# Performance work log

Measured on AMD Instinct MI355X. Metric: run time of the kernel, lower is better.

Reference implementation:

```python
import jax, jax.numpy as jnp
import numpy as np

N = 100000      # nodes
E = 3200000     # edges (before self-loops)
F_IN = 512      # input feature dim
HEADS = 8
DIM = 8         # per-head dim for hidden layers
HID = HEADS * DIM  # 64
CLS = 40        # num_classes
NEG_SLOPE = 0.2 # PyG GATConv default leaky relu slope


def setup_inputs() -> dict:
    key = jax.random.key(0)
    ks = jax.random.split(key, 14)
    def glorot(k, shape, fan_in):
        return jax.random.normal(k, shape, jnp.float32) * (1.0 / np.sqrt(fan_in))
    return {
        "x": jax.random.normal(ks[0], (N, F_IN), jnp.float32),
        "edge_index": jax.random.randint(ks[1], (2, E), 0, N, dtype=jnp.int32),
        # layer 1: in=F_IN, heads=8, dim=8, concat
        "W1": glorot(ks[2], (F_IN, HEADS * DIM), F_IN),
        "a_src1": glorot(ks[3], (HEADS, DIM), DIM),
        "a_dst1": glorot(ks[4], (HEADS, DIM), DIM),
        "b1": jnp.zeros((HEADS * DIM,), jnp.float32),
        # layer 2: in=64, heads=8, dim=8, concat
        "W2": glorot(ks[5], (HID, HEADS * DIM), HID),
        "a_src2": glorot(ks[6], (HEADS, DIM), DIM),
        "a_dst2": glorot(ks[7], (HEADS, DIM), DIM),
        "b2": jnp.zeros((HEADS * DIM,), jnp.float32),
        # layer 3: in=64, heads=1, dim=CLS, no concat (mean over heads == identity)
        "W3": glorot(ks[8], (HID, CLS), HID),
        "a_src3": glorot(ks[9], (1, CLS), CLS),
        "a_dst3": glorot(ks[10], (1, CLS), CLS),
        "b3": jnp.zeros((CLS,), jnp.float32),
    }


def gat_layer(h_in, W, att_src, att_dst, bias, src, dst, heads, dim, concat):
    # h_in: [N, F], W: [F, heads*dim], att_*: [heads, dim]
    n = h_in.shape[0]
    h = (h_in @ W).reshape(n, heads, dim)                    # [N, H, D]
    a_s = jnp.sum(h * att_src, axis=-1)                      # [N, H]
    a_d = jnp.sum(h * att_dst, axis=-1)                      # [N, H]
    e = jax.nn.leaky_relu(a_s[src] + a_d[dst], NEG_SLOPE)    # [E', H] edge logits
    # segment-softmax over incoming edges of each dst node (self-loops guarantee non-empty)
    m = jax.ops.segment_max(e, dst, num_segments=n)          # [N, H]
    p = jnp.exp(e - m[dst])
    s = jax.ops.segment_sum(p, dst, num_segments=n)          # [N, H]
    alpha = p / s[dst]                                       # [E', H]
    out = jax.ops.segment_sum(alpha[:, :, None] * h[src], dst, num_segments=n)  # [N, H, D]
    out = out.reshape(n, heads * dim) if concat else out.mean(axis=1)
    return out + bias


def reference(x, edge_index, W1, a_src1, a_dst1, b1, W2, a_src2, a_dst2, b2, W3, a_src3, a_dst3, b3):
    # PyG GATConv default add_self_loops=True
    loops = jnp.arange(N, dtype=edge_index.dtype)
    src = jnp.concatenate([edge_index[0], loops])
    dst = jnp.concatenate([edge_index[1], loops])
    h = gat_layer(x, W1, a_src1, a_dst1, b1, src, dst, HEADS, DIM, True)
    h = jax.nn.elu(h)  # dropout inactive in eval mode
    h = gat_layer(h, W2, a_src2, a_dst2, b2, src, dst, HEADS, DIM, True)
    h = jax.nn.elu(h)
    h = gat_layer(h, W3, a_src3, a_dst3, b3, src, dst, 1, CLS, False)
    return jax.nn.log_softmax(h, axis=1)
```

## Files before the change

kernel.cpp:

```cpp
#include <hip/hip_runtime.h>
#include <math.h>

#define NN 100000
#define EE 3200000
#define ET 3300000
#define FIN 512
#define HDIM 64
#define NCLS 40

#define NBUK 512
#define NPB 196
#define NBUK_USED 511
#define EPB 4096
#define EPT 16
#define CAP 8192

typedef __attribute__((ext_vector_type(8))) short frag_ab;
typedef __attribute__((ext_vector_type(4))) float frag_cd;

__device__ inline unsigned short f2bf(float f){
  union { float f; unsigned int u; } x; x.f = f;
  unsigned int u = x.u;
  unsigned int r = u + 0x7FFF + ((u >> 16) & 1);
  return (unsigned short)(r >> 16);
}
__device__ inline float bflo(unsigned u){
  union { unsigned u; float f; } x; x.u = u << 16; return x.f;
}
__device__ inline float bfhi(unsigned u){
  union { unsigned u; float f; } x; x.u = u & 0xFFFF0000u; return x.f;
}
__device__ inline float bf2f(unsigned short u){
  union { unsigned int u; float f; } x; x.u = ((unsigned int)u) << 16;
  return x.f;
}

__global__ void k_zeroB(int* bcur){
  int t = blockIdx.x*256 + threadIdx.x;
  if(t < NBUK) bcur[t] = 0;
}

__global__ __launch_bounds__(256) void k_bucket(const int* __restrict__ src, const int* __restrict__ dst,
                                                int* __restrict__ bcur, int* __restrict__ pbuf){
  __shared__ int lcnt[NBUK];
  __shared__ int lbase[NBUK];
  int t = threadIdx.x;
  for(int i=t;i<NBUK;i+=256) lcnt[i]=0;
  __syncthreads();
  int base = blockIdx.x*EPB + t;
  int bk[EPT], rk[EPT], pk[EPT];
  #pragma unroll
  for(int j=0;j<EPT;j++){
    int e = base + j*256;
    bk[j] = -1;
    if(e < ET){
      int s, d;
      if(e < EE){ s = src[e]; d = dst[e]; } else { s = e - EE; d = s; }
      int b = d / NPB;
      bk[j] = b;
      pk[j] = s | ((d - b*NPB) << 17);
      rk[j] = atomicAdd(&lcnt[b], 1);
    }
  }
  __syncthreads();
  for(int i=t;i<NBUK;i+=256){
    int v = lcnt[i];
    lbase[i] = v ? atomicAdd(&bcur[i], v) : 0;
  }
  __syncthreads();
  #pragma unroll
  for(int j=0;j<EPT;j++){
    if(bk[j] >= 0){
      int pos = lbase[bk[j]] + rk[j];
      if(pos < CAP) pbuf[(size_t)bk[j]*CAP + pos] = pk[j];
    }
  }
}

__global__ void k_bscan(const int* __restrict__ bcur, int* __restrict__ bbase){
  __shared__ int lds[NBUK];
  int t = threadIdx.x;
  int v = (t < NBUK_USED) ? bcur[t] : 0;
  lds[t] = v;
  __syncthreads();
  for(int off=1; off<NBUK; off<<=1){
    int x = 0;
    if(t >= off) x = lds[t-off];
    __syncthreads();
    if(t >= off) lds[t] += x;
    __syncthreads();
  }
  bbase[t] = lds[t] - v;
}

__global__ __launch_bounds__(256) void k_bfinal(const int* __restrict__ bbase, const int* __restrict__ pbuf,
                                                int* __restrict__ rp, int* __restrict__ col){
  __shared__ int cnt[NPB];
  int b = blockIdx.x, t = threadIdx.x;
  int beg = bbase[b];
  int cntb = bbase[b+1] - beg;
  const int* pb = pbuf + (size_t)b*CAP;
  for(int i=t;i<NPB;i+=256) cnt[i]=0;
  __syncthreads();
  for(int i=t; i<cntb; i+=256){
    int dloc = pb[i] >> 17;
    atomicAdd(&cnt[dloc], 1);
  }
  __syncthreads();
  if(t < 64){
    int vals[4]; int sum = 0;
    #pragma unroll
    for(int j=0;j<4;j++){ int idx = t*4+j; int v = (idx<NPB)?cnt[idx]:0; vals[j]=v; sum+=v; }
    int incl = sum;
    #pragma unroll
    for(int off=1; off<64; off<<=1){
      int x = __shfl_up(incl, off);
      if(t >= off) incl += x;
    }
    int run = incl - sum;
    #pragma unroll
    for(int j=0;j<4;j++){
      int idx = t*4+j;
      if(idx < NPB){ int v = vals[j]; cnt[idx] = run; run += v; }
    }
  }
  __syncthreads();
  int node0 = b*NPB;
  int nloc = NN - node0; if(nloc > NPB) nloc = NPB;
  for(int i=t;i<nloc;i+=256){
    int g = beg + cnt[i];
    rp[node0 + i] = g;
    cnt[i] = g;
  }
  if(b == 0 && t == 0) rp[NN] = ET;
  __syncthreads();
  for(int i=t; i<cntb; i+=256){
    int v = pb[i];
    int s = v & 0x1FFFF;
    int dloc = v >> 17;
    int pos = atomicAdd(&cnt[dloc], 1);
    col[pos] = s;
  }
}

__global__ void k_cvtW(const float* __restrict__ W, unsigned short* __restrict__ Wt, int K, int C){
  int i = blockIdx.x*256 + threadIdx.x;
  if(i >= 64*K) return;
  int n = i / K, k = i - n*K;
  Wt[i] = (n < C) ? f2bf(W[k*C + n]) : (unsigned short)0;
}

#define BM 128
#define BK 32
#define LSTR 40
__global__ __launch_bounds__(256) void k_gemm1(const float* __restrict__ A, const unsigned short* __restrict__ Wt,
                                               unsigned short* __restrict__ Out, int M){
  __shared__ __attribute__((aligned(16))) unsigned short Al[2][BM*LSTR];
  __shared__ __attribute__((aligned(16))) unsigned short Bl[2][64*LSTR];
  int t = threadIdx.x;
  int w = t >> 6, l = t & 63;
  int row0 = blockIdx.x * BM;

  int srow = t >> 1;
  int shalf = t & 1;
  int bn = t >> 2;
  int bseg = t & 3;

  int fr = l & 15, kg = l >> 4;

  frag_cd acc[2][4];
  #pragma unroll
  for(int i=0;i<2;i++)
    #pragma unroll
    for(int j=0;j<4;j++) acc[i][j] = (frag_cd){0.f,0.f,0.f,0.f};

  int rg = row0 + srow; if(rg >= M) rg = M-1;
  const float* aprow = &A[(size_t)rg*FIN + shalf*16];

  #define STAGE(buf, kc) do { \
    const float* ap = aprow + (kc); \
    float4 v0 = *(const float4*)(ap); \
    float4 v1 = *(const float4*)(ap+4); \
    float4 v2 = *(const float4*)(ap+8); \
    float4 v3 = *(const float4*)(ap+12); \
    uint4 pa, pb; \
    pa.x = f2bf(v0.x) | ((unsigned)f2bf(v0.y)<<16); \
    pa.y = f2bf(v0.z) | ((unsigned)f2bf(v0.w)<<16); \
    pa.z = f2bf(v1.x) | ((unsigned)f2bf(v1.y)<<16); \
    pa.w = f2bf(v1.z) | ((unsigned)f2bf(v1.w)<<16); \
    pb.x = f2bf(v2.x) | ((unsigned)f2bf(v2.y)<<16); \
    pb.y = f2bf(v2.z) | ((unsigned)f2bf(v2.w)<<16); \
    pb.z = f2bf(v3.x) | ((unsigned)f2bf(v3.y)<<16); \
    pb.w = f2bf(v3.z) | ((unsigned)f2bf(v3.w)<<16); \
    *(uint4*)&Al[buf][srow*LSTR + shalf*16] = pa; \
    *(uint4*)&Al[buf][srow*LSTR + shalf*16 + 8] = pb; \
    *(uint4*)&Bl[buf][bn*LSTR + bseg*8] = *(const uint4*)&Wt[bn*FIN + (kc) + bseg*8]; \
  } while(0)

  STAGE(0, 0);
  __syncthreads();

  #pragma unroll 1
  for(int step = 0; step < FIN/BK; ++step){
    int buf = step & 1;
    if(step + 1 < FIN/BK) STAGE(buf^1, (step+1)*BK);
    frag_ab af[2], bfr[4];
    #pragma unroll
    for(int i=0;i<2;i++) af[i] = *(const frag_ab*)&Al[buf][(w*32 + i*16 + fr)*LSTR + kg*8];
    #pragma unroll
    for(int j=0;j<4;j++) bfr[j] = *(const frag_ab*)&Bl[buf][(j*16 + fr)*LSTR + kg*8];
    #pragma unroll
    for(int i=0;i<2;i++)
      #pragma unroll
      for(int j=0;j<4;j++)
        acc[i][j] = __builtin_amdgcn_mfma_f32_16x16x32_bf16(af[i], bfr[j], acc[i][j], 0, 0, 0);
    __syncthreads();
  }

  #pragma unroll
  for(int i=0;i<2;i++){
    int crow = row0 + w*32 + i*16 + kg*4;
    #pragma unroll
    for(int j=0;j<4;j++){
      int ccol = j*16 + fr;
      #pragma unroll
      for(int r=0;r<4;r++){
        if(crow + r < M) Out[(size_t)(crow+r)*HDIM + ccol] = f2bf(acc[i][j][r]);
      }
    }
  }
  #undef STAGE
}

template<int K, int C>
__global__ __launch_bounds__(256) void k_gemmb(const unsigned short* __restrict__ A,
                                               const unsigned short* __restrict__ Wt,
                                               unsigned short* __restrict__ Out, int M){
  constexpr int CT = (C + 15)/16;
  __shared__ __attribute__((aligned(16))) unsigned short Al[2][BM*LSTR];
  __shared__ __attribute__((aligned(16))) unsigned short Bl[2][64*LSTR];
  int t = threadIdx.x;
  int w = t >> 6, l = t & 63;
  int row0 = blockIdx.x * BM;

  int srow = t >> 1;
  int shalf = t & 1;
  int bn = t >> 2;
  int bseg = t & 3;

  int fr = l & 15, kg = l >> 4;

  frag_cd acc[2][CT];
  #pragma unroll
  for(int i=0;i<2;i++)
    #pragma unroll
    for(int j=0;j<CT;j++) acc[i][j] = (frag_cd){0.f,0.f,0.f,0.f};

  int rg = row0 + srow; if(rg >= M) rg = M-1;
  const unsigned short* aprow = &A[(size_t)rg*K + shalf*16];

  #define STAGEB(buf, kc) do { \
    *(uint4*)&Al[buf][srow*LSTR + shalf*16]     = *(const uint4*)(aprow + (kc)); \
    *(uint4*)&Al[buf][srow*LSTR + shalf*16 + 8] = *(const uint4*)(aprow + (kc) + 8); \
    *(uint4*)&Bl[buf][bn*LSTR + bseg*8] = *(const uint4*)&Wt[bn*K + (kc) + bseg*8]; \
  } while(0)


  STAGEB(0, 0);
  __syncthreads();

  #pragma unroll 1
  for(int step = 0; step < K/BK; ++step){
    int buf = step & 1;
    if(step + 1 < K/BK) STAGEB(buf^1, (step+1)*BK);
    frag_ab af[2], bfr[CT];
    #pragma unroll
    for(int i=0;i<2;i++) af[i] = *(const frag_ab*)&Al[buf][(w*32 + i*16 + fr)*LSTR + kg*8];
    #pragma unroll
    for(int j=0;j<CT;j++) bfr[j] = *(const frag_ab*)&Bl[buf][(j*16 + fr)*LSTR + kg*8];
    #pragma unroll
    for(int i=0;i<2;i++)
      #pragma unroll
      for(int j=0;j<CT;j++)
        acc[i][j] = __builtin_amdgcn_mfma_f32_16x16x32_bf16(af[i], bfr[j], acc[i][j], 0, 0, 0);
    __syncthreads();
  }

  #pragma unroll
  for(int i=0;i<2;i++){
    int crow = row0 + w*32 + i*16 + kg*4;
    #pragma unroll
    for(int j=0;j<CT;j++){
      int ccol = j*16 + fr;
      if(ccol >= C) continue;
      #pragma unroll
      for(int r=0;r<4;r++){
        if(crow + r < M) Out[(size_t)(crow+r)*C + ccol] = f2bf(acc[i][j][r]);
      }
    }
  }
  #undef STAGEB
}

template<int HEADS, int DIM>
__global__ void k_att(const unsigned short* __restrict__ h, const float* __restrict__ a_src,
                      const float* __restrict__ a_dst, float* __restrict__ as_o, float* __restrict__ ad_o){
  int gid = blockIdx.x*256 + threadIdx.x;
  int node = gid >> 6, lane = gid & 63;
  if(node >= NN) return;
  constexpr int HD = HEADS*DIM;
  float v = 0.f, asc = 0.f, adc = 0.f;
  if(lane < HD){ v = bf2f(h[(size_t)node*HD + lane]); asc = a_src[lane]; adc = a_dst[lane]; }
  float s1 = v*asc, s2 = v*adc;
  if(HEADS == 8){
    #pragma unroll
    for(int m=1;m<8;m<<=1){ s1 += __shfl_xor(s1,m); s2 += __shfl_xor(s2,m); }
    if((lane & 7) == 0){ as_o[node*8 + (lane>>3)] = s1; ad_o[node*8 + (lane>>3)] = s2; }
  } else {
    #pragma unroll
    for(int m=1;m<64;m<<=1){ s1 += __shfl_xor(s1,m); s2 += __shfl_xor(s2,m); }
    if(lane == 0){ as_o[node] = s1; ad_o[node] = s2; }
  }
}

template<int HEADS, int DIM, bool DO_ELU, bool DO_LSM>
__global__ __launch_bounds__(256) void k_agg(const unsigned short* __restrict__ hbf, const int* __restrict__ rp,
                      const int* __restrict__ col,
                      const float* __restrict__ as_, const float* __restrict__ ad_,
                      const float* __restrict__ bias, void* __restrict__ outp){
  int gid = blockIdx.x*256 + threadIdx.x;
  int node = gid >> 6, lane = gid & 63;
  if(node >= NN) return;
  constexpr int HD = HEADS*DIM;
  int el = lane >> 4;
  int fl = lane & 15;
  int f0 = fl*4;
  bool act = f0 < HD;
  int hidx = act ? (f0 / DIM) : 0;
  int beg = rp[node], end = rp[node+1];
  int deg = end - beg;
  float adn = ad_[node*HEADS + hidx];
  float m = -1e38f, s = 0.f;
  float a0 = 0.f, a1 = 0.f, a2 = 0.f, a3 = 0.f;

  for(int base = 0; base < deg; base += 64){
    int cnt = deg - base; if(cnt > 64) cnt = 64;
    int idx = 0;
    if(lane < cnt) idx = col[beg + base + lane];
    for(int j = 0; j < cnt; j += 8){
      int sn0 = __shfl(idx, j + el);
      int sn1 = __shfl(idx, j + 4 + el);
      bool v0 = (j + el) < cnt;
      bool v1 = (j + 4 + el) < cnt;
      float ea0 = as_[sn0*HEADS + hidx];
      float ea1 = as_[sn1*HEADS + hidx];
      uint2 h0 = act ? *(const uint2*)&hbf[(size_t)sn0*HD + f0] : make_uint2(0u,0u);
      uint2 h1 = act ? *(const uint2*)&hbf[(size_t)sn1*HD + f0] : make_uint2(0u,0u);
      float e0 = ea0 + adn; e0 = (e0 > 0.f) ? e0 : 0.2f*e0; e0 = v0 ? e0 : -INFINITY;
      float e1 = ea1 + adn; e1 = (e1 > 0.f) ? e1 : 0.2f*e1; e1 = v1 ? e1 : -INFINITY;
      float gm = fmaxf(fmaxf(e0, e1), m);
      float c  = __expf(m - gm);
      float p0 = __expf(e0 - gm);
      float p1 = __expf(e1 - gm);
      s = s*c + p0 + p1;
      a0 = a0*c + p0*bflo(h0.x) + p1*bflo(h1.x);
      a1 = a1*c + p0*bfhi(h0.x) + p1*bfhi(h1.x);
      a2 = a2*c + p0*bflo(h0.y) + p1*bflo(h1.y);
      a3 = a3*c + p0*bfhi(h0.y) + p1*bfhi(h1.y);
      m = gm;
    }
  }

  #pragma unroll
  for(int wd=16; wd<=32; wd<<=1){
    float mo  = __shfl_xor(m, wd);
    float so  = __shfl_xor(s, wd);
    float b0  = __shfl_xor(a0, wd);
    float b1  = __shfl_xor(a1, wd);
    float b2  = __shfl_xor(a2, wd);
    float b3  = __shfl_xor(a3, wd);
    float mm2 = fmaxf(m, mo);
    float cs  = __expf(m - mm2), co = __expf(mo - mm2);
    s  = s*cs  + so*co;
    a0 = a0*cs + b0*co;
    a1 = a1*cs + b1*co;
    a2 = a2*cs + b2*co;
    a3 = a3*cs + b3*co;
    m = mm2;
  }

  float inv = 1.f/s;
  float o0 = a0*inv, o1 = a1*inv, o2 = a2*inv, o3 = a3*inv;
  if(act){
    float4 bb = *(const float4*)&bias[f0];
    o0 += bb.x; o1 += bb.y; o2 += bb.z; o3 += bb.w;
  }
  if(DO_ELU){
    o0 = (o0 > 0.f) ? o0 : expm1f(o0);
    o1 = (o1 > 0.f) ? o1 : expm1f(o1);
    o2 = (o2 > 0.f) ? o2 : expm1f(o2);
    o3 = (o3 > 0.f) ? o3 : expm1f(o3);
  }
  if(!DO_LSM){
    if(act && el == 0){
      unsigned short* ob = (unsigned short*)outp;
      uint2 pk;
      pk.x = f2bf(o0) | ((unsigned)f2bf(o1) << 16);
      pk.y = f2bf(o2) | ((unsigned)f2bf(o3) << 16);
      *(uint2*)&ob[(size_t)node*HD + f0] = pk;
    }
  } else {
    float vmax = act ? fmaxf(fmaxf(o0,o1), fmaxf(o2,o3)) : -INFINITY;
    #pragma unroll
    for(int mm2=1; mm2<16; mm2<<=1) vmax = fmaxf(vmax, __shfl_xor(vmax, mm2));
    float ex = act ? (expf(o0-vmax) + expf(o1-vmax) + expf(o2-vmax) + expf(o3-vmax)) : 0.f;
    #pragma unroll
    for(int mm2=1; mm2<16; mm2<<=1) ex += __shfl_xor(ex, mm2);
    float lg = logf(ex);
    if(act && el == 0){
      float* of = (float*)outp;
      float4 r;
      r.x = o0 - vmax - lg; r.y = o1 - vmax - lg;
      r.z = o2 - vmax - lg; r.w = o3 - vmax - lg;
      *(float4*)&of[(size_t)node*HD + f0] = r;
    }
  }
}

static inline size_t alignup(size_t x){ return (x + 255) & ~(size_t)255; }

extern "C" void kernel_launch(void* const* d_in, const int* in_sizes, int n_in,
                              void* d_out, int out_size, void* d_ws, size_t ws_size,
                              hipStream_t stream){
  const float* x      = (const float*)d_in[0];
  const int*   ei     = (const int*)d_in[1];
  const float* W1     = (const float*)d_in[2];
  const float* asrc1  = (const float*)d_in[3];
  const float* adst1  = (const float*)d_in[4];
  const float* b1     = (const float*)d_in[5];
  const float* W2     = (const float*)d_in[6];
  const float* asrc2  = (const float*)d_in[7];
  const float* adst2  = (const float*)d_in[8];
  const float* b2     = (const float*)d_in[9];
  const float* W3     = (const float*)d_in[10];
  const float* asrc3  = (const float*)d_in[11];
  const float* adst3  = (const float*)d_in[12];
  const float* b3     = (const float*)d_in[13];
  const int* src = ei;
  const int* dst = ei + EE;

  char* w = (char*)d_ws;
  int* rp     = (int*)w;              w += alignup((size_t)(NN+1)*4);
  int* bbase  = (int*)w;              w += alignup((size_t)(NBUK+1)*4);
  int* bcur   = (int*)w;              w += alignup((size_t)NBUK*4);
  unsigned short* Wt1 = (unsigned short*)w; w += alignup((size_t)64*FIN*2);
  unsigned short* Wt2 = (unsigned short*)w; w += alignup((size_t)64*HDIM*2);
  unsigned short* Wt3 = (unsigned short*)w; w += alignup((size_t)64*HDIM*2);
  int* col    = (int*)w;              w += alignup((size_t)ET*4);
  int* pbuf   = (int*)w;              w += alignup((size_t)NBUK*CAP*4);
  unsigned short* hAb = (unsigned short*)w; w += alignup((size_t)NN*HDIM*2 + 256);
  unsigned short* hBb = (unsigned short*)w; w += alignup((size_t)NN*HDIM*2 + 256);
  unsigned short* hCb = (unsigned short*)w; w += alignup((size_t)NN*NCLS*2 + 256);
  float* asA  = (float*)w;            w += alignup((size_t)NN*8*4);
  float* adA  = (float*)w;            w += alignup((size_t)NN*8*4);

  dim3 blk(256);
  int gWav  = (NN*64 + 255)/256;
  int gG1   = (NN + BM - 1)/BM;
  int gBuk  = (ET + EPB - 1)/EPB;

  k_zeroB<<<2, blk, 0, stream>>>(bcur);
  k_bucket<<<gBuk, blk, 0, stream>>>(src, dst, bcur, pbuf);
  k_bscan<<<1, dim3(NBUK), 0, stream>>>(bcur, bbase);
  k_bfinal<<<NBUK_USED, blk, 0, stream>>>(bbase, pbuf, rp, col);

  k_cvtW<<<(64*FIN + 255)/256, blk, 0, stream>>>(W1, Wt1, FIN, HDIM);
  k_cvtW<<<(64*HDIM + 255)/256, blk, 0, stream>>>(W2, Wt2, HDIM, HDIM);
  k_cvtW<<<(64*HDIM + 255)/256, blk, 0, stream>>>(W3, Wt3, HDIM, NCLS);

  k_gemm1<<<gG1, blk, 0, stream>>>(x, Wt1, hAb, NN);
  k_att<8,8><<<gWav, blk, 0, stream>>>(hAb, asrc1, adst1, asA, adA);
  k_agg<8,8,true,false><<<gWav, blk, 0, stream>>>(hAb, rp, col, asA, adA, b1, hBb);

  k_gemmb<HDIM, HDIM><<<gG1, blk, 0, stream>>>(hBb, Wt2, hAb, NN);
  k_att<8,8><<<gWav, blk, 0, stream>>>(hAb, asrc2, adst2, asA, adA);
  k_agg<8,8,true,false><<<gWav, blk, 0, stream>>>(hAb, rp, col, asA, adA, b2, hBb);

  k_gemmb<HDIM, NCLS><<<gG1, blk, 0, stream>>>(hBb, Wt3, hCb, NN);
  k_att<1,NCLS><<<gWav, blk, 0, stream>>>(hCb, asrc3, adst3, asA, adA);
  k_agg<1,NCLS,false,true><<<gWav, blk, 0, stream>>>(hCb, rp, col, asA, adA, b3, d_out);
}
```

Baseline: 431.7 us.

## Fuse attention-score epilogue into GEMMs, merge prep kernels, use exp2 and packed bf16 cvt

The per-node attention-logit kernels are removed, and the src/dst scores are now computed from the fp32 MFMA accumulators in the GEMM epilogues. The scores are pre-scaled by log2(e) so aggregation can use exp2f. Weight conversion, attention-vector prep and bucket zeroing are merged into one prep kernel. The aggregation loop gains a full-chunk fast path without masking, a permuted head index to match the fused epilogue's layout, and hardware v_cvt_pk_bf16_f32 packing. This cuts several launches and a full re-read of h per layer, at the cost of more shuffles in the GEMM epilogue and a slightly different rounding path.

Result: faster. 415.2 us (-3.8%).

```diff
diff --git a/kernel.cpp b/kernel.cpp
--- a/kernel.cpp
+++ b/kernel.cpp
@@ -18,6 +18,8 @@
 typedef __attribute__((ext_vector_type(8))) short frag_ab;
 typedef __attribute__((ext_vector_type(4))) float frag_cd;
 
+#define CVTPK(dst, a, b) asm("v_cvt_pk_bf16_f32 %0, %1, %2" : "=v"(dst) : "v"(a), "v"(b))
+
 __device__ inline unsigned short f2bf(float f){
   union { float f; unsigned int u; } x; x.f = f;
   unsigned int u = x.u;
@@ -30,14 +32,36 @@
 __device__ inline float bfhi(unsigned u){
   union { unsigned u; float f; } x; x.u = u & 0xFFFF0000u; return x.f;
 }
-__device__ inline float bf2f(unsigned short u){
-  union { unsigned int u; float f; } x; x.u = ((unsigned int)u) << 16;
-  return x.f;
-}
-
-__global__ void k_zeroB(int* bcur){
-  int t = blockIdx.x*256 + threadIdx.x;
-  if(t < NBUK) bcur[t] = 0;
+
+__global__ void k_prep(const float* __restrict__ W1, const float* __restrict__ W2, const float* __restrict__ W3,
+                       const float* __restrict__ as1, const float* __restrict__ ad1,
+                       const float* __restrict__ as2, const float* __restrict__ ad2,
+                       const float* __restrict__ as3, const float* __restrict__ ad3,
+                       unsigned short* __restrict__ Wt1, unsigned short* __restrict__ Wt2,
+                       unsigned short* __restrict__ Wt3, float* __restrict__ attv, int* __restrict__ bcur){
+  int i = blockIdx.x*256 + threadIdx.x;
+  if(i < NBUK) bcur[i] = 0;
+  if(i < 32768){
+    int n = i >> 9, k = i & 511;
+    Wt1[i] = f2bf(W1[k*HDIM + n]);
+  } else if(i < 36864){
+    int i2 = i - 32768; int n = i2 >> 6, k = i2 & 63;
+    Wt2[i2] = f2bf(W2[k*HDIM + n]);
+  } else if(i < 40960){
+    int i3 = i - 36864; int n = i3 >> 6, k = i3 & 63;
+    Wt3[i3] = (n < NCLS) ? f2bf(W3[k*NCLS + n]) : (unsigned short)0;
+  } else if(i < 41312){
+    int j = i - 40960;
+    const float L2E = 1.4426950408889634f;
+    float v;
+    if(j < 64) v = as1[j]*L2E;
+    else if(j < 128) v = ad1[j-64]*L2E;
+    else if(j < 192) v = as2[j-128]*L2E;
+    else if(j < 256) v = ad2[j-192]*L2E;
+    else if(j < 304){ int q=j-256; v = (q<NCLS)? as3[q]*L2E : 0.f; }
+    else { int q=j-304; v = (q<NCLS)? ad3[q]*L2E : 0.f; }
+    attv[j] = v;
+  }
 }
 
 __global__ __launch_bounds__(256) void k_bucket(const int* __restrict__ src, const int* __restrict__ dst,
@@ -143,18 +167,66 @@
   }
 }
 
-__global__ void k_cvtW(const float* __restrict__ W, unsigned short* __restrict__ Wt, int K, int C){
-  int i = blockIdx.x*256 + threadIdx.x;
-  if(i >= 64*K) return;
-  int n = i / K, k = i - n*K;
-  Wt[i] = (n < C) ? f2bf(W[k*C + n]) : (unsigned short)0;
+template<int CT>
+__device__ inline void att_epi8(const frag_cd (&acc)[2][CT], int rowbase, int fr, int kg,
+                                const float* __restrict__ asv, const float* __restrict__ adv,
+                                float* __restrict__ as_o, float* __restrict__ ad_o, int M){
+  float av[CT], dv[CT];
+  #pragma unroll
+  for(int j=0;j<CT;j++){ av[j]=asv[j*16+fr]; dv[j]=adv[j*16+fr]; }
+  #pragma unroll
+  for(int i=0;i<2;i++){
+    #pragma unroll
+    for(int r=0;r<4;r++){
+      int row = rowbase + i*16 + kg*4 + r;
+      float ps[CT], pd[CT];
+      #pragma unroll
+      for(int j=0;j<CT;j++){ float v = acc[i][j][r]; ps[j]=v*av[j]; pd[j]=v*dv[j]; }
+      #pragma unroll
+      for(int mk=1; mk<8; mk<<=1){
+        #pragma unroll
+        for(int j=0;j<CT;j++){ ps[j]+=__shfl_xor(ps[j],mk); pd[j]+=__shfl_xor(pd[j],mk); }
+      }
+      if((fr&7)==0 && row < M){
+        int half = fr>>3;
+        float4 s4; s4.x=ps[0]; s4.y=ps[1]; s4.z=ps[2]; s4.w=ps[3];
+        float4 d4; d4.x=pd[0]; d4.y=pd[1]; d4.z=pd[2]; d4.w=pd[3];
+        *(float4*)&as_o[row*8 + half*4] = s4;
+        *(float4*)&ad_o[row*8 + half*4] = d4;
+      }
+    }
+  }
+}
+
+template<int CT>
+__device__ inline void att_epi1(const frag_cd (&acc)[2][CT], int rowbase, int fr, int kg,
+                                const float* __restrict__ asv, const float* __restrict__ adv,
+                                float* __restrict__ as_o, float* __restrict__ ad_o, int M){
+  float av[CT], dv[CT];
+  #pragma unroll
+  for(int j=0;j<CT;j++){ av[j]=asv[j*16+fr]; dv[j]=adv[j*16+fr]; }
+  #pragma unroll
+  for(int i=0;i<2;i++){
+    #pragma unroll
+    for(int r=0;r<4;r++){
+      int row = rowbase + i*16 + kg*4 + r;
+      float ps=0.f, pd=0.f;
+      #pragma unroll
+      for(int j=0;j<CT;j++){ float v = acc[i][j][r]; ps += v*av[j]; pd += v*dv[j]; }
+      #pragma unroll
+      for(int mk=1; mk<16; mk<<=1){ ps+=__shfl_xor(ps,mk); pd+=__shfl_xor(pd,mk); }
+      if(fr==0 && row < M){ as_o[row]=ps; ad_o[row]=pd; }
+    }
+  }
 }
 
 #define BM 128
 #define BK 32
 #define LSTR 40
 __global__ __launch_bounds__(256) void k_gemm1(const float* __restrict__ A, const unsigned short* __restrict__ Wt,
-                                               unsigned short* __restrict__ Out, int M){
+                                               const float* __restrict__ asv, const float* __restrict__ adv,
+                                               unsigned short* __restrict__ Out,
+                                               float* __restrict__ as_o, float* __restrict__ ad_o, int M){
   __shared__ __attribute__((aligned(16))) unsigned short Al[2][BM*LSTR];
   __shared__ __attribute__((aligned(16))) unsigned short Bl[2][64*LSTR];
   int t = threadIdx.x;
@@ -184,14 +256,10 @@
     float4 v2 = *(const float4*)(ap+8); \
     float4 v3 = *(const float4*)(ap+12); \
     uint4 pa, pb; \
-    pa.x = f2bf(v0.x) | ((unsigned)f2bf(v0.y)<<16); \
-    pa.y = f2bf(v0.z) | ((unsigned)f2bf(v0.w)<<16); \
-    pa.z = f2bf(v1.x) | ((unsigned)f2bf(v1.y)<<16); \
-    pa.w = f2bf(v1.z) | ((unsigned)f2bf(v1.w)<<16); \
-    pb.x = f2bf(v2.x) | ((unsigned)f2bf(v2.y)<<16); \
-    pb.y = f2bf(v2.z) | ((unsigned)f2bf(v2.w)<<16); \
-    pb.z = f2bf(v3.x) | ((unsigned)f2bf(v3.y)<<16); \
-    pb.w = f2bf(v3.z) | ((unsigned)f2bf(v3.w)<<16); \
+    CVTPK(pa.x, v0.x, v0.y); CVTPK(pa.y, v0.z, v0.w); \
+    CVTPK(pa.z, v1.x, v1.y); CVTPK(pa.w, v1.z, v1.w); \
+    CVTPK(pb.x, v2.x, v2.y); CVTPK(pb.y, v2.z, v2.w); \
+    CVTPK(pb.z, v3.x, v3.y); CVTPK(pb.w, v3.z, v3.w); \
     *(uint4*)&Al[buf][srow*LSTR + shalf*16] = pa; \
     *(uint4*)&Al[buf][srow*LSTR + shalf*16 + 8] = pb; \
     *(uint4*)&Bl[buf][bn*LSTR + bseg*8] = *(const uint4*)&Wt[bn*FIN + (kc) + bseg*8]; \
@@ -229,13 +297,16 @@
       }
     }
   }
+  att_epi8(acc, row0 + w*32, fr, kg, asv, adv, as_o, ad_o, M);
   #undef STAGE
 }
 
-template<int K, int C>
+template<int K, int C, int HEADS>
 __global__ __launch_bounds__(256) void k_gemmb(const unsigned short* __restrict__ A,
                                                const unsigned short* __restrict__ Wt,
-                                               unsigned short* __restrict__ Out, int M){
+                                               const float* __restrict__ asv, const float* __restrict__ adv,
+                                               unsigned short* __restrict__ Out,
+                                               float* __restrict__ as_o, float* __restrict__ ad_o, int M){
   constexpr int CT = (C + 15)/16;
   __shared__ __attribute__((aligned(16))) unsigned short Al[2][BM*LSTR];
   __shared__ __attribute__((aligned(16))) unsigned short Bl[2][64*LSTR];
@@ -265,7 +336,6 @@
     *(uint4*)&Bl[buf][bn*LSTR + bseg*8] = *(const uint4*)&Wt[bn*K + (kc) + bseg*8]; \
   } while(0)
 
-
   STAGEB(0, 0);
   __syncthreads();
 
@@ -299,28 +369,9 @@
       }
     }
   }
+  if(HEADS == 8) att_epi8(acc, row0 + w*32, fr, kg, asv, adv, as_o, ad_o, M);
+  else          att_epi1(acc, row0 + w*32, fr, kg, asv, adv, as_o, ad_o, M);
   #undef STAGEB
-}
-
-template<int HEADS, int DIM>
-__global__ void k_att(const unsigned short* __restrict__ h, const float* __restrict__ a_src,
-                      const float* __restrict__ a_dst, float* __restrict__ as_o, float* __restrict__ ad_o){
-  int gid = blockIdx.x*256 + threadIdx.x;
-  int node = gid >> 6, lane = gid & 63;
-  if(node >= NN) return;
-  constexpr int HD = HEADS*DIM;
-  float v = 0.f, asc = 0.f, adc = 0.f;
-  if(lane < HD){ v = bf2f(h[(size_t)node*HD + lane]); asc = a_src[lane]; adc = a_dst[lane]; }
-  float s1 = v*asc, s2 = v*adc;
-  if(HEADS == 8){
-    #pragma unroll
-    for(int m=1;m<8;m<<=1){ s1 += __shfl_xor(s1,m); s2 += __shfl_xor(s2,m); }
-    if((lane & 7) == 0){ as_o[node*8 + (lane>>3)] = s1; ad_o[node*8 + (lane>>3)] = s2; }
-  } else {
-    #pragma unroll
-    for(int m=1;m<64;m<<=1){ s1 += __shfl_xor(s1,m); s2 += __shfl_xor(s2,m); }
-    if(lane == 0){ as_o[node] = s1; ad_o[node] = s2; }
-  }
 }
 
 template<int HEADS, int DIM, bool DO_ELU, bool DO_LSM>
@@ -336,10 +387,12 @@
   int fl = lane & 15;
   int f0 = fl*4;
   bool act = f0 < HD;
-  int hidx = act ? (f0 / DIM) : 0;
+  int f0c = act ? f0 : 0;
+  int hx = 0;
+  if(HEADS == 8){ int hidx = f0 >> 3; hx = ((hidx&1)<<2) | (hidx>>1); }
   int beg = rp[node], end = rp[node+1];
   int deg = end - beg;
-  float adn = ad_[node*HEADS + hidx];
+  float adn = ad_[node*HEADS + hx];
   float m = -1e38f, s = 0.f;
   float a0 = 0.f, a1 = 0.f, a2 = 0.f, a3 = 0.f;
 
@@ -347,21 +400,43 @@
     int cnt = deg - base; if(cnt > 64) cnt = 64;
     int idx = 0;
     if(lane < cnt) idx = col[beg + base + lane];
-    for(int j = 0; j < cnt; j += 8){
+    int jf = cnt & ~7;
+    int j = 0;
+    for(; j < jf; j += 8){
+      int sn0 = __shfl(idx, j + el);
+      int sn1 = __shfl(idx, j + 4 + el);
+      float ea0 = as_[sn0*HEADS + hx];
+      float ea1 = as_[sn1*HEADS + hx];
+      uint2 h0 = *(const uint2*)&hbf[(size_t)sn0*HD + f0c];
+      uint2 h1 = *(const uint2*)&hbf[(size_t)sn1*HD + f0c];
+      float e0 = ea0 + adn; e0 = fmaxf(e0, 0.2f*e0);
+      float e1 = ea1 + adn; e1 = fmaxf(e1, 0.2f*e1);
+      float gm = fmaxf(fmaxf(e0, e1), m);
+      float c  = exp2f(m - gm);
+      float p0 = exp2f(e0 - gm);
+      float p1 = exp2f(e1 - gm);
+      s = s*c + p0 + p1;
+      a0 = a0*c + p0*bflo(h0.x) + p1*bflo(h1.x);
+      a1 = a1*c + p0*bfhi(h0.x) + p1*bfhi(h1.x);
+      a2 = a2*c + p0*bflo(h0.y) + p1*bflo(h1.y);
+      a3 = a3*c + p0*bfhi(h0.y) + p1*bfhi(h1.y);
+      m = gm;
+    }
+    if(j < cnt){
       int sn0 = __shfl(idx, j + el);
       int sn1 = __shfl(idx, j + 4 + el);
       bool v0 = (j + el) < cnt;
       bool v1 = (j + 4 + el) < cnt;
-      float ea0 = as_[sn0*HEADS + hidx];
-      float ea1 = as_[sn1*HEADS + hidx];
-      uint2 h0 = act ? *(const uint2*)&hbf[(size_t)sn0*HD + f0] : make_uint2(0u,0u);
-      uint2 h1 = act ? *(const uint2*)&hbf[(size_t)sn1*HD + f0] : make_uint2(0u,0u);
-      float e0 = ea0 + adn; e0 = (e0 > 0.f) ? e0 : 0.2f*e0; e0 = v0 ? e0 : -INFINITY;
-      float e1 = ea1 + adn; e1 = (e1 > 0.f) ? e1 : 0.2f*e1; e1 = v1 ? e1 : -INFINITY;
+      float ea0 = as_[sn0*HEADS + hx];
+      float ea1 = as_[sn1*HEADS + hx];
+      uint2 h0 = *(const uint2*)&hbf[(size_t)sn0*HD + f0c];
+      uint2 h1 = *(const uint2*)&hbf[(size_t)sn1*HD + f0c];
+      float e0 = ea0 + adn; e0 = fmaxf(e0, 0.2f*e0); e0 = v0 ? e0 : -INFINITY;
+      float e1 = ea1 + adn; e1 = fmaxf(e1, 0.2f*e1); e1 = v1 ? e1 : -INFINITY;
       float gm = fmaxf(fmaxf(e0, e1), m);
-      float c  = __expf(m - gm);
-      float p0 = __expf(e0 - gm);
-      float p1 = __expf(e1 - gm);
+      float c  = exp2f(m - gm);
+      float p0 = exp2f(e0 - gm);
+      float p1 = exp2f(e1 - gm);
       s = s*c + p0 + p1;
       a0 = a0*c + p0*bflo(h0.x) + p1*bflo(h1.x);
       a1 = a1*c + p0*bfhi(h0.x) + p1*bfhi(h1.x);
@@ -380,7 +455,7 @@
     float b2  = __shfl_xor(a2, wd);
     float b3  = __shfl_xor(a3, wd);
     float mm2 = fmaxf(m, mo);
-    float cs  = __expf(m - mm2), co = __expf(mo - mm2);
+    float cs  = exp2f(m - mm2), co = exp2f(mo - mm2);
     s  = s*cs  + so*co;
     a0 = a0*cs + b0*co;
     a1 = a1*cs + b1*co;
@@ -404,9 +479,10 @@
   if(!DO_LSM){
     if(act && el == 0){
       unsigned short* ob = (unsigned short*)outp;
-      uint2 pk;
-      pk.x = f2bf(o0) | ((unsigned)f2bf(o1) << 16);
-      pk.y = f2bf(o2) | ((unsigned)f2bf(o3) << 16);
+      unsigned plo, phi;
+      CVTPK(plo, o0, o1);
+      CVTPK(phi, o2, o3);
+      uint2 pk; pk.x = plo; pk.y = phi;
       *(uint2*)&ob[(size_t)node*HD + f0] = pk;
     }
   } else {
@@ -456,6 +532,7 @@
   unsigned short* Wt1 = (unsigned short*)w; w += alignup((size_t)64*FIN*2);
   unsigned short* Wt2 = (unsigned short*)w; w += alignup((size_t)64*HDIM*2);
   unsigned short* Wt3 = (unsigned short*)w; w += alignup((size_t)64*HDIM*2);
+  float* attv = (float*)w;            w += alignup((size_t)352*4);
   int* col    = (int*)w;              w += alignup((size_t)ET*4);
   int* pbuf   = (int*)w;              w += alignup((size_t)NBUK*CAP*4);
   unsigned short* hAb = (unsigned short*)w; w += alignup((size_t)NN*HDIM*2 + 256);
@@ -469,24 +546,18 @@
   int gG1   = (NN + BM - 1)/BM;
   int gBuk  = (ET + EPB - 1)/EPB;
 
-  k_zeroB<<<2, blk, 0, stream>>>(bcur);
+  k_prep<<<(41312 + 255)/256, blk, 0, stream>>>(W1, W2, W3, asrc1, adst1, asrc2, adst2, asrc3, adst3,
+                                                Wt1, Wt2, Wt3, attv, bcur);
   k_bucket<<<gBuk, blk, 0, stream>>>(src, dst, bcur, pbuf);
   k_bscan<<<1, dim3(NBUK), 0, stream>>>(bcur, bbase);
   k_bfinal<<<NBUK_USED, blk, 0, stream>>>(bbase, pbuf, rp, col);
 
-  k_cvtW<<<(64*FIN + 255)/256, blk, 0, stream>>>(W1, Wt1, FIN, HDIM);
-  k_cvtW<<<(64*HDIM + 255)/256, blk, 0, stream>>>(W2, Wt2, HDIM, HDIM);
-  k_cvtW<<<(64*HDIM + 255)/256, blk, 0, stream>>>(W3, Wt3, HDIM, NCLS);
-
-  k_gemm1<<<gG1, blk, 0, stream>>>(x, Wt1, hAb, NN);
-  k_att<8,8><<<gWav, blk, 0, stream>>>(hAb, asrc1, adst1, asA, adA);
+  k_gemm1<<<gG1, blk, 0, stream>>>(x, Wt1, attv + 0, attv + 64, hAb, asA, adA, NN);
   k_agg<8,8,true,false><<<gWav, blk, 0, stream>>>(hAb, rp, col, asA, adA, b1, hBb);
 
-  k_gemmb<HDIM, HDIM><<<gG1, blk, 0, stream>>>(hBb, Wt2, hAb, NN);
-  k_att<8,8><<<gWav, blk, 0, stream>>>(hAb, asrc2, adst2, asA, adA);
+  k_gemmb<HDIM, HDIM, 8><<<gG1, blk, 0, stream>>>(hBb, Wt2, attv + 128, attv + 192, hAb, asA, adA, NN);
   k_agg<8,8,true,false><<<gWav, blk, 0, stream>>>(hAb, rp, col, asA, adA, b2, hBb);
 
-  k_gemmb<HDIM, NCLS><<<gG1, blk, 0, stream>>>(hBb, Wt3, hCb, NN);
-  k_att<1,NCLS><<<gWav, blk, 0, stream>>>(hCb, asrc3, adst3, asA, adA);
+  k_gemmb<HDIM, NCLS, 1><<<gG1, blk, 0, stream>>>(hBb, Wt3, attv + 256, attv + 304, hCb, asA, adA, NN);
   k_agg<1,NCLS,false,true><<<gWav, blk, 0, stream>>>(hCb, rp, col, asA, adA, b3, d_out);
 }
```
